# Kernel tuning notes

Hardware: AMD Instinct MI355X
Metric: run time of the kernel (lower is better)

## Reference

```python
import jax, jax.numpy as jnp
import numpy as np

T, H, E, I, K = 2048, 2048, 8, 2048, 2


def setup_inputs() -> dict:
    key = jax.random.key(0)
    ks = jax.random.split(key, 6)
    s_in = 1.0 / np.sqrt(H)
    s_mid = 1.0 / np.sqrt(I)
    return {
        "hidden_states": jax.random.normal(ks[0], (T, H), jnp.float32),
        "router_logits": jax.random.normal(ks[1], (T, E), jnp.float32),
        "per_expert_scale": jax.random.uniform(ks[2], (E,), jnp.float32, 0.5, 1.5),
        "w_gate": jax.random.normal(ks[3], (E, H, I), jnp.float32) * s_in,
        "w_up": jax.random.normal(ks[4], (E, H, I), jnp.float32) * s_in,
        "w_down": jax.random.normal(ks[5], (E, I, H), jnp.float32) * s_mid,
    }


def _route(router_logits, per_expert_scale):
    # Gemma4 routing: topk over logits, softmax over ALL experts,
    # renormalize over selected experts, fold in per-expert scale.
    _, topk_ids = jax.lax.top_k(router_logits, K)              # [T, K]
    probs = jax.nn.softmax(router_logits, axis=-1)             # [T, E]
    topk_probs = jnp.take_along_axis(probs, topk_ids, axis=-1)  # [T, K]
    renorm = jnp.sum(topk_probs, axis=-1, keepdims=True)
    renorm = jnp.where(renorm > 0.0, renorm, 1.0)
    topk_weights = topk_probs / renorm
    topk_weights = topk_weights * per_expert_scale[topk_ids]
    return topk_weights.astype(jnp.float32), topk_ids.astype(jnp.int32)


def reference(hidden_states, router_logits, per_expert_scale, w_gate, w_up, w_down):
    topk_weights, topk_ids = _route(router_logits, per_expert_scale)
    # dense combine weights [T, E] (zero outside top-k slots)
    combine = jnp.zeros((T, E), jnp.float32)
    combine = combine.at[jnp.arange(T)[:, None], topk_ids].set(topk_weights)
    # gated gelu MLP per expert, dense over experts, weighted combine
    g = jax.nn.gelu(jnp.einsum('th,ehi->tei', hidden_states, w_gate), approximate=True)
    u = jnp.einsum('th,ehi->tei', hidden_states, w_up)
    expert_out = jnp.einsum('tei,eih->teh', g * u, w_down)      # [T, E, H]
    out = jnp.einsum('te,teh->th', combine, expert_out)
    return out
```

## Files before the change

### kernel.cpp

```cpp
#include <hip/hip_runtime.h>
#include <hip/hip_bf16.h>

#define TT 2048
#define HD 2048
#define ID 2048
#define NE 8

typedef __attribute__((ext_vector_type(8))) short short8;
typedef __attribute__((ext_vector_type(4))) float f4;

__device__ __forceinline__ unsigned short b16(float f){
  union { __hip_bfloat16 b; unsigned short u; } x;
  x.b = __float2bfloat16(f);
  return x.u;
}
__device__ __forceinline__ unsigned pk2(float lo, float hi){
  return (unsigned)b16(lo) | ((unsigned)b16(hi) << 16);
}
__device__ __forceinline__ float gelu_t(float x){
  float y = 0.7978845608028654f * (x + 0.044715f * x * x * x);
  float t = 1.0f - 2.0f / (__expf(2.0f * y) + 1.0f);
  return 0.5f * x * (1.0f + t);
}
__device__ __forceinline__ void glds16(const void* g, void* l){
  __builtin_amdgcn_global_load_lds(
      (const __attribute__((address_space(1))) unsigned*)g,
      (__attribute__((address_space(3))) unsigned*)l, 16, 0, 0);
}
__device__ __forceinline__ void softbar(){
  asm volatile("s_waitcnt lgkmcnt(0)" ::: "memory");
  __builtin_amdgcn_s_barrier();
  __builtin_amdgcn_sched_barrier(0);
}
__device__ __forceinline__ int swzB2(int np){ return (((np >> 2) & 7) ^ ((np & 3) << 1)) & 7; }

__global__ void k_cvtx(const float* __restrict__ X, __hip_bfloat16* __restrict__ Xb){
  int i = blockIdx.x * 256 + threadIdx.x;
  const f4* src = (const f4*)X + (size_t)i * 2;
  f4 a = src[0], b = src[1];
  uint4 o = { pk2(a[0],a[1]), pk2(a[2],a[3]), pk2(b[0],b[1]), pk2(b[2],b[3]) };
  ((uint4*)Xb)[i] = o;
}

__global__ void k_route(const float* __restrict__ lg, const float* __restrict__ sc,
                        int* __restrict__ rid, float* __restrict__ rw){
  int t = blockIdx.x * blockDim.x + threadIdx.x;
  if (t >= TT) return;
  float l[NE];
#pragma unroll
  for (int e = 0; e < NE; e++) l[e] = lg[t * NE + e];
  float mx = l[0];
#pragma unroll
  for (int e = 1; e < NE; e++) mx = fmaxf(mx, l[e]);
  float p[NE];
#pragma unroll
  for (int e = 0; e < NE; e++) p[e] = __expf(l[e] - mx);
  int i0 = 0; float b0 = l[0];
#pragma unroll
  for (int e = 1; e < NE; e++) if (l[e] > b0){ b0 = l[e]; i0 = e; }
  int i1 = -1; float b1 = -1e30f;
#pragma unroll
  for (int e = 0; e < NE; e++) if (e != i0 && l[e] > b1){ b1 = l[e]; i1 = e; }
  float p0 = p[i0], p1 = p[i1];
  float rn = p0 + p1; rn = (rn > 0.f) ? rn : 1.f;
  rw[t*2]   = p0 / rn * sc[i0];
  rw[t*2+1] = p1 / rn * sc[i1];
  rid[t*2]  = i0;
  rid[t*2+1]= i1;
}

__global__ void k_lists(const int* __restrict__ rid, const float* __restrict__ rw,
                        int* __restrict__ row_tok, float* __restrict__ row_w,
                        int* __restrict__ off){
  int lane = threadIdx.x;
  int ids[64]; float wv[64];
#pragma unroll
  for (int i = 0; i < 64; i++) ids[i] = rid[i * 64 + lane];
#pragma unroll
  for (int i = 0; i < 64; i++) wv[i] = rw[i * 64 + lane];
  int cnt[NE];
#pragma unroll
  for (int e = 0; e < NE; e++) cnt[e] = 0;
#pragma unroll
  for (int i = 0; i < 64; i++){
#pragma unroll
    for (int e = 0; e < NE; e++)
      cnt[e] += __popcll(__ballot(ids[i] == e));
  }
  int offs[NE + 1]; offs[0] = 0;
#pragma unroll
  for (int e = 0; e < NE; e++) offs[e + 1] = offs[e] + cnt[e];
  if (lane == 0){
#pragma unroll
    for (int e = 0; e <= NE; e++) off[e] = offs[e];
  }
  int run[NE];
#pragma unroll
  for (int e = 0; e < NE; e++) run[e] = offs[e];
  unsigned long long ltm = (1ULL << lane) - 1ULL;
#pragma unroll
  for (int i = 0; i < 64; i++){
    int id = ids[i];
    int tok = (i * 64 + lane) >> 1;
#pragma unroll
    for (int e = 0; e < NE; e++){
      unsigned long long m = __ballot(id == e);
      if (id == e){
        int pos = run[e] + __popcll(m & ltm);
        row_tok[pos] = tok;
        row_w[pos]   = wv[i];
      }
      run[e] += __popcll(m);
    }
  }
}


__global__ __launch_bounds__(256, 3)
void k_gu_f(const __hip_bfloat16* __restrict__ Xb, const float* __restrict__ Wg,
            const float* __restrict__ Wu, const int* __restrict__ row_tok,
            const int* __restrict__ off, __hip_bfloat16* __restrict__ hbuf){
  __shared__ __align__(16) char sA[16384];
  __shared__ __align__(16) char sB[16384];
  __shared__ int s_tok[128];

  const int bid = blockIdx.x;
  const int e  = bid & 7;
  const int t  = bid >> 3;
  const int mt = t % 5;
  const int nt = t / 5;
  const int o0 = off[e], cnt = off[e + 1] - o0;
  if (mt * 128 >= cnt) return;
  const int p0 = o0 + mt * 128;
  const int cntL = min(128, cnt - mt * 128);
  const int tid = threadIdx.x;
  const int wid = tid >> 6, lane = tid & 63;

  if (tid < 128) s_tok[tid] = row_tok[min(p0 + tid, TT*2 - 1)];
  __syncthreads();

  const int sw = (((lane & 7) ^ (lane >> 3)) & 7) << 4;
  const char* asrc[4];
#pragma unroll
  for (int i = 0; i < 4; i++){
    int r = (wid * 4 + i) * 8 + (lane >> 3);
    asrc[i] = (const char*)Xb + (size_t)s_tok[r] * 4096 + sw;
  }
  const int m2 = tid >> 7, tt = tid & 127;
  const int n0 = (tt & 15) * 4;
  const int k0 = (tt >> 4) * 4;
  const float* wsrc = (m2 ? Wu : Wg) + (size_t)e * HD * ID
                    + (size_t)k0 * ID + (size_t)nt * 64 + n0;
  int bw0[4], bw1[4];
#pragma unroll
  for (int j = 0; j < 4; j++){
    int n  = n0 + j;
    int np = (n >> 5) * 64 + (n & 31) + m2 * 32;
    int s0 = k0 >> 3;
    int sub = (k0 & 4) << 1;
    int F  = swzB2(np);
    bw0[j] = np * 128 + (((s0      ^ F) & 7) << 4) + sub;
    bw1[j] = np * 128 + (((s0 ^ 4  ^ F) & 7) << 4) + sub;
  }
  const int wm = wid >> 1, wn = wid & 1;
  const int kg = lane >> 4, ln = lane & 15;
  int aoff[4], boff[4];
#pragma unroll
  for (int f = 0; f < 4; f++){
    int m = wm * 64 + f * 16 + ln;
    aoff[f] = m * 128 + (((kg ^ (m & 7)) & 7) << 4);
    int n = wn * 64 + f * 16 + ln;
    boff[f] = n * 128 + (((kg ^ swzB2(n)) & 7) << 4);
  }

  f4 acc[4][4];
#pragma unroll
  for (int a = 0; a < 4; a++)
#pragma unroll
    for (int b = 0; b < 4; b++) acc[a][b] = f4{0,0,0,0};

  f4 r0, r1, r2, r3, r4, r5, r6, r7;
  { const float* p = wsrc;
    r0 = *(const f4*)(p);          r1 = *(const f4*)(p + ID);
    r2 = *(const f4*)(p + 2*ID);   r3 = *(const f4*)(p + 3*ID);
    r4 = *(const f4*)(p + 32*ID);  r5 = *(const f4*)(p + 33*ID);
    r6 = *(const f4*)(p + 34*ID);  r7 = *(const f4*)(p + 35*ID); }

  for (int kt = 0; kt < 32; ++kt){
    softbar();
#pragma unroll
    for (int j = 0; j < 4; j++){
      *(uint2*)(sB + bw0[j]) = uint2{ pk2(r0[j], r1[j]), pk2(r2[j], r3[j]) };
      *(uint2*)(sB + bw1[j]) = uint2{ pk2(r4[j], r5[j]), pk2(r6[j], r7[j]) };
    }
    __builtin_amdgcn_sched_barrier(0);
    { const int _o = kt * 128;
#pragma unroll
      for (int i = 0; i < 4; i++) glds16(asrc[i] + _o, sA + (wid * 4 + i) * 1024);
    }
    __builtin_amdgcn_sched_barrier(0);
    if (kt + 1 < 32){
      const float* p = wsrc + (size_t)(kt + 1) * 64 * ID;
      r0 = *(const f4*)(p);          r1 = *(const f4*)(p + ID);
      r2 = *(const f4*)(p + 2*ID);   r3 = *(const f4*)(p + 3*ID);
      r4 = *(const f4*)(p + 32*ID);  r5 = *(const f4*)(p + 33*ID);
      r6 = *(const f4*)(p + 34*ID);  r7 = *(const f4*)(p + 35*ID);
    }
    __builtin_amdgcn_sched_barrier(0);
    if (kt + 1 < 32){
      asm volatile("s_waitcnt vmcnt(8) lgkmcnt(0)" ::: "memory");
    } else {
      asm volatile("s_waitcnt vmcnt(0) lgkmcnt(0)" ::: "memory");
    }
    __builtin_amdgcn_s_barrier();
    __builtin_amdgcn_sched_barrier(0);
#pragma unroll
    for (int ks = 0; ks < 2; ks++){
      const int kx = ks * 64;
      short8 af[4], bf[4];
#pragma unroll
      for (int f = 0; f < 4; f++) af[f] = *(const short8*)(sA + (aoff[f] ^ kx));
#pragma unroll
      for (int f = 0; f < 4; f++) bf[f] = *(const short8*)(sB + (boff[f] ^ kx));
#pragma unroll
      for (int fn = 0; fn < 4; fn++)
#pragma unroll
        for (int fm = 0; fm < 4; fm++)
          acc[fm][fn] = __builtin_amdgcn_mfma_f32_16x16x32_bf16(af[fm], bf[fn], acc[fm][fn], 0, 0, 0);
    }
  }
#pragma unroll
  for (int fm = 0; fm < 4; fm++){
#pragma unroll
    for (int r = 0; r < 4; r++){
      int row = wm * 64 + fm * 16 + (lane >> 4) * 4 + r;
      if (row < cntL){
        size_t base = (size_t)(p0 + row) * ID + (size_t)nt * 64 + wn * 32 + ln;
#pragma unroll
        for (int fn = 0; fn < 2; fn++){
          float g = acc[fm][fn][r];
          float u = acc[fm][fn + 2][r];
          hbuf[base + fn * 16] = __float2bfloat16(gelu_t(g) * u);
        }
      }
    }
  }
}

__global__ __launch_bounds__(256, 3)
void k_dn_f(const __hip_bfloat16* __restrict__ hbuf, const float* __restrict__ Wd,
            const int* __restrict__ row_tok, const float* __restrict__ row_w,
            const int* __restrict__ off, float* __restrict__ out){
  __shared__ __align__(16) char sA[16384];
  __shared__ __align__(16) char sB[16384];
  __shared__ int s_tok[128];
  __shared__ float s_w[128];

  const int bid = blockIdx.x;
  const int e  = bid & 7;
  const int t  = bid >> 3;
  const int mt = t % 5;
  const int nt = t / 5;
  const int o0 = off[e], cnt = off[e + 1] - o0;
  if (mt * 128 >= cnt) return;
  const int p0 = o0 + mt * 128;
  const int cntL = min(128, cnt - mt * 128);
  const int tid = threadIdx.x;
  const int wid = tid >> 6, lane = tid & 63;

  if (tid < 128){
    int p = min(p0 + tid, TT*2 - 1);
    s_tok[tid] = row_tok[p];
    s_w[tid]   = row_w[p];
  }
  __syncthreads();

  const int sw = (((lane & 7) ^ (lane >> 3)) & 7) << 4;
  const char* asrc[4];
#pragma unroll
  for (int i = 0; i < 4; i++){
    int r = (wid * 4 + i) * 8 + (lane >> 3);
    int p = min(p0 + r, TT*2 - 1);
    asrc[i] = (const char*)hbuf + (size_t)p * 4096 + sw;
  }
  const int n0 = (tid & 31) * 4;
  const int k0 = (tid >> 5) * 4;
  const float* wsrc = Wd + (size_t)e * ID * HD + (size_t)k0 * HD + (size_t)nt * 128 + n0;
  int bw0[4], bw1[4];
#pragma unroll
  for (int j = 0; j < 4; j++){
    int np = n0 + j;
    int s0 = k0 >> 3;
    int sub = (k0 & 4) << 1;
    int F  = swzB2(np);
    bw0[j] = np * 128 + (((s0     ^ F) & 7) << 4) + sub;
    bw1[j] = np * 128 + (((s0 ^ 4 ^ F) & 7) << 4) + sub;
  }
  const int wm = wid >> 1, wn = wid & 1;
  const int kg = lane >> 4, ln = lane & 15;
  int aoff[4], boff[4];
#pragma unroll
  for (int f = 0; f < 4; f++){
    int m = wm * 64 + f * 16 + ln;
    aoff[f] = m * 128 + (((kg ^ (m & 7)) & 7) << 4);
    int n = wn * 64 + f * 16 + ln;
    boff[f] = n * 128 + (((kg ^ swzB2(n)) & 7) << 4);
  }

  f4 acc[4][4];
#pragma unroll
  for (int a = 0; a < 4; a++)
#pragma unroll
    for (int b = 0; b < 4; b++) acc[a][b] = f4{0,0,0,0};

  f4 r0, r1, r2, r3, r4, r5, r6, r7;
  { const float* p = wsrc;
    r0 = *(const f4*)(p);          r1 = *(const f4*)(p + HD);
    r2 = *(const f4*)(p + 2*HD);   r3 = *(const f4*)(p + 3*HD);
    r4 = *(const f4*)(p + 32*HD);  r5 = *(const f4*)(p + 33*HD);
    r6 = *(const f4*)(p + 34*HD);  r7 = *(const f4*)(p + 35*HD); }

  for (int kt = 0; kt < 32; ++kt){
    softbar();
#pragma unroll
    for (int j = 0; j < 4; j++){
      *(uint2*)(sB + bw0[j]) = uint2{ pk2(r0[j], r1[j]), pk2(r2[j], r3[j]) };
      *(uint2*)(sB + bw1[j]) = uint2{ pk2(r4[j], r5[j]), pk2(r6[j], r7[j]) };
    }
    __builtin_amdgcn_sched_barrier(0);
    { const int _o = kt * 128;
#pragma unroll
      for (int i = 0; i < 4; i++) glds16(asrc[i] + _o, sA + (wid * 4 + i) * 1024);
    }
    __builtin_amdgcn_sched_barrier(0);
    if (kt + 1 < 32){
      const float* p = wsrc + (size_t)(kt + 1) * 64 * HD;
      r0 = *(const f4*)(p);          r1 = *(const f4*)(p + HD);
      r2 = *(const f4*)(p + 2*HD);   r3 = *(const f4*)(p + 3*HD);
      r4 = *(const f4*)(p + 32*HD);  r5 = *(const f4*)(p + 33*HD);
      r6 = *(const f4*)(p + 34*HD);  r7 = *(const f4*)(p + 35*HD);
    }
    __builtin_amdgcn_sched_barrier(0);
    if (kt + 1 < 32){
      asm volatile("s_waitcnt vmcnt(8) lgkmcnt(0)" ::: "memory");
    } else {
      asm volatile("s_waitcnt vmcnt(0) lgkmcnt(0)" ::: "memory");
    }
    __builtin_amdgcn_s_barrier();
    __builtin_amdgcn_sched_barrier(0);
#pragma unroll
    for (int ks = 0; ks < 2; ks++){
      const int kx = ks * 64;
      short8 af[4], bf[4];
#pragma unroll
      for (int f = 0; f < 4; f++) af[f] = *(const short8*)(sA + (aoff[f] ^ kx));
#pragma unroll
      for (int f = 0; f < 4; f++) bf[f] = *(const short8*)(sB + (boff[f] ^ kx));
#pragma unroll
      for (int fn = 0; fn < 4; fn++)
#pragma unroll
        for (int fm = 0; fm < 4; fm++)
          acc[fm][fn] = __builtin_amdgcn_mfma_f32_16x16x32_bf16(af[fm], bf[fn], acc[fm][fn], 0, 0, 0);
    }
  }
#pragma unroll
  for (int fm = 0; fm < 4; fm++){
#pragma unroll
    for (int r = 0; r < 4; r++){
      int row = wm * 64 + fm * 16 + (lane >> 4) * 4 + r;
      if (row < cntL){
        int tok = s_tok[row];
        float w = s_w[row];
        float* ob = out + (size_t)tok * HD + (size_t)nt * 128 + wn * 64 + ln;
#pragma unroll
        for (int fn = 0; fn < 4; fn++)
          atomicAdd(ob + fn * 16, acc[fm][fn][r] * w);
      }
    }
  }
}

extern "C" void kernel_launch(void* const* d_in, const int* in_sizes, int n_in,
                              void* d_out, int out_size, void* d_ws, size_t ws_size,
                              hipStream_t stream){
  (void)in_sizes; (void)n_in; (void)out_size; (void)ws_size;
  const float* X  = (const float*)d_in[0];
  const float* RL = (const float*)d_in[1];
  const float* SC = (const float*)d_in[2];
  const float* Wg = (const float*)d_in[3];
  const float* Wu = (const float*)d_in[4];
  const float* Wd = (const float*)d_in[5];
  float* out = (float*)d_out;

  char* ws = (char*)d_ws;
  int*   rid     = (int*)(ws);
  float* rw      = (float*)(ws + 16384);
  int*   row_tok = (int*)(ws + 32768);
  float* row_w   = (float*)(ws + 49152);
  int*   off     = (int*)(ws + 65536);
  __hip_bfloat16* hbuf = (__hip_bfloat16*)(ws + 66560);
  __hip_bfloat16* Xb   = (__hip_bfloat16*)(ws + 66560 + 16777216ull);

  hipMemsetAsync(d_out, 0, (size_t)TT * HD * sizeof(float), stream);
  k_cvtx <<<2048, 256, 0, stream>>>(X, Xb);
  k_route<<<TT / 256, 256, 0, stream>>>(RL, SC, rid, rw);
  k_lists<<<1, 64, 0, stream>>>(rid, rw, row_tok, row_w, off);
  k_gu_f<<<1280, 256, 0, stream>>>(Xb, Wg, Wu, row_tok, off, hbuf);
  k_dn_f<<< 640, 256, 0, stream>>>(hbuf, Wd, row_tok, row_w, off, out);
}
```

Baseline: 313.7 us.

## Double-buffer activation tile in LDS and widen weight staging to 16-byte stores

In both the gate/up and down expert GEMM kernels, the activation (A) tile now lives in two LDS buffers, so the global-to-LDS copy for step kt+1 is issued while step kt computes. Each thread now loads 8 consecutive k-rows of weights instead of two 4-row groups, which lets it pack them into one 16-byte LDS store per column. The explicit vmcnt wait is dropped and ordering relies on compiler-inserted waits on the weight registers. The cost is a larger LDS footprint per block, which could limit the three-blocks-per-CU occupancy target, and correctness now depends on that implicit memory ordering.

```diff
diff --git a/kernel.cpp b/kernel.cpp
--- a/kernel.cpp
+++ b/kernel.cpp
@@ -120,7 +120,7 @@
 void k_gu_f(const __hip_bfloat16* __restrict__ Xb, const float* __restrict__ Wg,
             const float* __restrict__ Wu, const int* __restrict__ row_tok,
             const int* __restrict__ off, __hip_bfloat16* __restrict__ hbuf){
-  __shared__ __align__(16) char sA[16384];
+  __shared__ __align__(16) char sA[2][16384];
   __shared__ __align__(16) char sB[16384];
   __shared__ int s_tok[128];
 
@@ -148,19 +148,15 @@
   }
   const int m2 = tid >> 7, tt = tid & 127;
   const int n0 = (tt & 15) * 4;
-  const int k0 = (tt >> 4) * 4;
+  const int s0 = tt >> 4;
   const float* wsrc = (m2 ? Wu : Wg) + (size_t)e * HD * ID
-                    + (size_t)k0 * ID + (size_t)nt * 64 + n0;
-  int bw0[4], bw1[4];
+                    + (size_t)(s0 * 8) * ID + (size_t)nt * 64 + n0;
+  int bw[4];
 #pragma unroll
   for (int j = 0; j < 4; j++){
     int n  = n0 + j;
     int np = (n >> 5) * 64 + (n & 31) + m2 * 32;
-    int s0 = k0 >> 3;
-    int sub = (k0 & 4) << 1;
-    int F  = swzB2(np);
-    bw0[j] = np * 128 + (((s0      ^ F) & 7) << 4) + sub;
-    bw1[j] = np * 128 + (((s0 ^ 4  ^ F) & 7) << 4) + sub;
+    bw[j] = np * 128 + (((s0 ^ swzB2(np)) & 7) << 4);
   }
   const int wm = wid >> 1, wn = wid & 1;
   const int kg = lane >> 4, ln = lane & 15;
@@ -179,47 +175,43 @@
 #pragma unroll
     for (int b = 0; b < 4; b++) acc[a][b] = f4{0,0,0,0};
 
-  f4 r0, r1, r2, r3, r4, r5, r6, r7;
-  { const float* p = wsrc;
-    r0 = *(const f4*)(p);          r1 = *(const f4*)(p + ID);
-    r2 = *(const f4*)(p + 2*ID);   r3 = *(const f4*)(p + 3*ID);
-    r4 = *(const f4*)(p + 32*ID);  r5 = *(const f4*)(p + 33*ID);
-    r6 = *(const f4*)(p + 34*ID);  r7 = *(const f4*)(p + 35*ID); }
+#pragma unroll
+  for (int i = 0; i < 4; i++) glds16(asrc[i], &sA[0][0] + (wid * 4 + i) * 1024);
+  f4 rk[8];
+#pragma unroll
+  for (int i = 0; i < 8; i++) rk[i] = *(const f4*)(wsrc + (size_t)i * ID);
 
   for (int kt = 0; kt < 32; ++kt){
     softbar();
 #pragma unroll
     for (int j = 0; j < 4; j++){
-      *(uint2*)(sB + bw0[j]) = uint2{ pk2(r0[j], r1[j]), pk2(r2[j], r3[j]) };
-      *(uint2*)(sB + bw1[j]) = uint2{ pk2(r4[j], r5[j]), pk2(r6[j], r7[j]) };
-    }
-    __builtin_amdgcn_sched_barrier(0);
-    { const int _o = kt * 128;
-#pragma unroll
-      for (int i = 0; i < 4; i++) glds16(asrc[i] + _o, sA + (wid * 4 + i) * 1024);
+      *(uint4*)(sB + bw[j]) = uint4{ pk2(rk[0][j], rk[1][j]), pk2(rk[2][j], rk[3][j]),
+                                     pk2(rk[4][j], rk[5][j]), pk2(rk[6][j], rk[7][j]) };
+    }
+    __builtin_amdgcn_sched_barrier(0);
+    if (kt + 1 < 32){
+      const int _o = (kt + 1) * 128;
+      char* dst = &sA[(kt + 1) & 1][0] + (wid * 4) * 1024;
+#pragma unroll
+      for (int i = 0; i < 4; i++) glds16(asrc[i] + _o, dst + i * 1024);
     }
     __builtin_amdgcn_sched_barrier(0);
     if (kt + 1 < 32){
       const float* p = wsrc + (size_t)(kt + 1) * 64 * ID;
-      r0 = *(const f4*)(p);          r1 = *(const f4*)(p + ID);
-      r2 = *(const f4*)(p + 2*ID);   r3 = *(const f4*)(p + 3*ID);
-      r4 = *(const f4*)(p + 32*ID);  r5 = *(const f4*)(p + 33*ID);
-      r6 = *(const f4*)(p + 34*ID);  r7 = *(const f4*)(p + 35*ID);
-    }
-    __builtin_amdgcn_sched_barrier(0);
-    if (kt + 1 < 32){
-      asm volatile("s_waitcnt vmcnt(8) lgkmcnt(0)" ::: "memory");
-    } else {
-      asm volatile("s_waitcnt vmcnt(0) lgkmcnt(0)" ::: "memory");
-    }
+#pragma unroll
+      for (int i = 0; i < 8; i++) rk[i] = *(const f4*)(p + (size_t)i * ID);
+    }
+    __builtin_amdgcn_sched_barrier(0);
+    asm volatile("s_waitcnt lgkmcnt(0)" ::: "memory");
     __builtin_amdgcn_s_barrier();
     __builtin_amdgcn_sched_barrier(0);
+    const char* A = &sA[kt & 1][0];
 #pragma unroll
     for (int ks = 0; ks < 2; ks++){
       const int kx = ks * 64;
       short8 af[4], bf[4];
 #pragma unroll
-      for (int f = 0; f < 4; f++) af[f] = *(const short8*)(sA + (aoff[f] ^ kx));
+      for (int f = 0; f < 4; f++) af[f] = *(const short8*)(A + (aoff[f] ^ kx));
 #pragma unroll
       for (int f = 0; f < 4; f++) bf[f] = *(const short8*)(sB + (boff[f] ^ kx));
 #pragma unroll
@@ -251,7 +243,7 @@
 void k_dn_f(const __hip_bfloat16* __restrict__ hbuf, const float* __restrict__ Wd,
             const int* __restrict__ row_tok, const float* __restrict__ row_w,
             const int* __restrict__ off, float* __restrict__ out){
-  __shared__ __align__(16) char sA[16384];
+  __shared__ __align__(16) char sA[2][16384];
   __shared__ __align__(16) char sB[16384];
   __shared__ int s_tok[128];
   __shared__ float s_w[128];
@@ -284,17 +276,13 @@
     asrc[i] = (const char*)hbuf + (size_t)p * 4096 + sw;
   }
   const int n0 = (tid & 31) * 4;
-  const int k0 = (tid >> 5) * 4;
-  const float* wsrc = Wd + (size_t)e * ID * HD + (size_t)k0 * HD + (size_t)nt * 128 + n0;
-  int bw0[4], bw1[4];
+  const int s0 = tid >> 5;
+  const float* wsrc = Wd + (size_t)e * ID * HD + (size_t)(s0 * 8) * HD + (size_t)nt * 128 + n0;
+  int bw[4];
 #pragma unroll
   for (int j = 0; j < 4; j++){
     int np = n0 + j;
-    int s0 = k0 >> 3;
-    int sub = (k0 & 4) << 1;
-    int F  = swzB2(np);
-    bw0[j] = np * 128 + (((s0     ^ F) & 7) << 4) + sub;
-    bw1[j] = np * 128 + (((s0 ^ 4 ^ F) & 7) << 4) + sub;
+    bw[j] = np * 128 + (((s0 ^ swzB2(np)) & 7) << 4);
   }
   const int wm = wid >> 1, wn = wid & 1;
   const int kg = lane >> 4, ln = lane & 15;
@@ -313,47 +301,43 @@
 #pragma unroll
     for (int b = 0; b < 4; b++) acc[a][b] = f4{0,0,0,0};
 
-  f4 r0, r1, r2, r3, r4, r5, r6, r7;
-  { const float* p = wsrc;
-    r0 = *(const f4*)(p);          r1 = *(const f4*)(p + HD);
-    r2 = *(const f4*)(p + 2*HD);   r3 = *(const f4*)(p + 3*HD);
-    r4 = *(const f4*)(p + 32*HD);  r5 = *(const f4*)(p + 33*HD);
-    r6 = *(const f4*)(p + 34*HD);  r7 = *(const f4*)(p + 35*HD); }
+#pragma unroll
+  for (int i = 0; i < 4; i++) glds16(asrc[i], &sA[0][0] + (wid * 4 + i) * 1024);
+  f4 rk[8];
+#pragma unroll
+  for (int i = 0; i < 8; i++) rk[i] = *(const f4*)(wsrc + (size_t)i * HD);
 
   for (int kt = 0; kt < 32; ++kt){
     softbar();
 #pragma unroll
     for (int j = 0; j < 4; j++){
-      *(uint2*)(sB + bw0[j]) = uint2{ pk2(r0[j], r1[j]), pk2(r2[j], r3[j]) };
-      *(uint2*)(sB + bw1[j]) = uint2{ pk2(r4[j], r5[j]), pk2(r6[j], r7[j]) };
-    }
-    __builtin_amdgcn_sched_barrier(0);
-    { const int _o = kt * 128;
-#pragma unroll
-      for (int i = 0; i < 4; i++) glds16(asrc[i] + _o, sA + (wid * 4 + i) * 1024);
+      *(uint4*)(sB + bw[j]) = uint4{ pk2(rk[0][j], rk[1][j]), pk2(rk[2][j], rk[3][j]),
+                                     pk2(rk[4][j], rk[5][j]), pk2(rk[6][j], rk[7][j]) };
+    }
+    __builtin_amdgcn_sched_barrier(0);
+    if (kt + 1 < 32){
+      const int _o = (kt + 1) * 128;
+      char* dst = &sA[(kt + 1) & 1][0] + (wid * 4) * 1024;
+#pragma unroll
+      for (int i = 0; i < 4; i++) glds16(asrc[i] + _o, dst + i * 1024);
     }
     __builtin_amdgcn_sched_barrier(0);
     if (kt + 1 < 32){
       const float* p = wsrc + (size_t)(kt + 1) * 64 * HD;
-      r0 = *(const f4*)(p);          r1 = *(const f4*)(p + HD);
-      r2 = *(const f4*)(p + 2*HD);   r3 = *(const f4*)(p + 3*HD);
-      r4 = *(const f4*)(p + 32*HD);  r5 = *(const f4*)(p + 33*HD);
-      r6 = *(const f4*)(p + 34*HD);  r7 = *(const f4*)(p + 35*HD);
-    }
-    __builtin_amdgcn_sched_barrier(0);
-    if (kt + 1 < 32){
-      asm volatile("s_waitcnt vmcnt(8) lgkmcnt(0)" ::: "memory");
-    } else {
-      asm volatile("s_waitcnt vmcnt(0) lgkmcnt(0)" ::: "memory");
-    }
+#pragma unroll
+      for (int i = 0; i < 8; i++) rk[i] = *(const f4*)(p + (size_t)i * HD);
+    }
+    __builtin_amdgcn_sched_barrier(0);
+    asm volatile("s_waitcnt lgkmcnt(0)" ::: "memory");
     __builtin_amdgcn_s_barrier();
     __builtin_amdgcn_sched_barrier(0);
+    const char* A = &sA[kt & 1][0];
 #pragma unroll
     for (int ks = 0; ks < 2; ks++){
       const int kx = ks * 64;
       short8 af[4], bf[4];
 #pragma unroll
-      for (int f = 0; f < 4; f++) af[f] = *(const short8*)(sA + (aoff[f] ^ kx));
+      for (int f = 0; f < 4; f++) af[f] = *(const short8*)(A + (aoff[f] ^ kx));
 #pragma unroll
       for (int f = 0; f < 4; f++) bf[f] = *(const short8*)(sB + (boff[f] ^ kx));
 #pragma unroll
```

Result: faster. 305.0 us (-2.8%).
